# Kernel optimization log

Measured on AMD Instinct MI355X. Metric: run time of the kernel, lower is better.

Reference implementation:

```python
import jax, jax.numpy as jnp
import numpy as np

N = 100000
E = 1000000
F = 64
H = 64
G = 64  # number of graphs
EPS = 1e-5


def setup_inputs() -> dict:
    key = jax.random.key(0)
    ks = jax.random.split(key, 12)
    x = jax.random.normal(ks[0], (N, F), dtype=jnp.float32)
    edge_index = jax.random.randint(ks[1], (2, E), 0, N, dtype=jnp.int32)
    batch = jnp.sort(jax.random.randint(ks[2], (N,), 0, G, dtype=jnp.int32))
    s1 = 1.0 / np.sqrt(F)
    s2 = 1.0 / np.sqrt(H)
    inp = {
        "x": x,
        "edge_index": edge_index,
        "batch": batch,
        # GCNConv layers (weight [out,in] like torch Linear, bias [out])
        "W1": jax.random.uniform(ks[3], (H, F), jnp.float32, -s1, s1),
        "b1": jnp.zeros((H,), jnp.float32),
        "W2": jax.random.uniform(ks[4], (H, H), jnp.float32, -s2, s2),
        "b2": jnp.zeros((H,), jnp.float32),
        # BatchNorm (eval mode: running stats)
        "bn1_g": jnp.ones((H,), jnp.float32),
        "bn1_b": jnp.zeros((H,), jnp.float32),
        "bn1_m": jax.random.normal(ks[5], (H,), jnp.float32) * 0.1,
        "bn1_v": jax.random.uniform(ks[6], (H,), jnp.float32, 0.5, 1.5),
        "bn2_g": jnp.ones((H,), jnp.float32),
        "bn2_b": jnp.zeros((H,), jnp.float32),
        "bn2_m": jax.random.normal(ks[7], (H,), jnp.float32) * 0.1,
        "bn2_v": jax.random.uniform(ks[8], (H,), jnp.float32, 0.5, 1.5),
        # MLP head
        "lin1_W": jax.random.uniform(ks[9], (H // 2, H), jnp.float32, -s2, s2),
        "lin1_b": jnp.zeros((H // 2,), jnp.float32),
        "lin2_W": jax.random.uniform(ks[10], (1, H // 2), jnp.float32, -1.0 / np.sqrt(H // 2), 1.0 / np.sqrt(H // 2)),
        "lin2_b": jnp.zeros((1,), jnp.float32),
    }
    return inp


def _gcn_norm(edge_index):
    # PyG GCNConv default: add self-loops, symmetric normalization
    loop = jnp.arange(N, dtype=edge_index.dtype)
    row = jnp.concatenate([edge_index[0], loop])  # source
    col = jnp.concatenate([edge_index[1], loop])  # target
    deg = jax.ops.segment_sum(jnp.ones_like(col, jnp.float32), col, num_segments=N)
    dinv = jnp.where(deg > 0, jax.lax.rsqrt(deg), 0.0)
    norm = dinv[row] * dinv[col]  # [E+N]
    return row, col, norm


def _gcn_conv(x, W, b, row, col, norm):
    h = x @ W.T                       # [N, H] transform first (cheap)
    msg = h[row] * norm[:, None]      # [E+N, H] gather + scale
    out = jax.ops.segment_sum(msg, col, num_segments=N)  # scatter-add
    return out + b


def _bn_eval(x, g, b, m, v):
    return (x - m) * (g * jax.lax.rsqrt(v + EPS)) + b


def reference(x, edge_index, batch, W1, b1, W2, b2,
              bn1_g, bn1_b, bn1_m, bn1_v, bn2_g, bn2_b, bn2_m, bn2_v,
              lin1_W, lin1_b, lin2_W, lin2_b):
    row, col, norm = _gcn_norm(edge_index)
    # layer 1: conv -> BN -> relu (dropout inactive in eval)
    h = _gcn_conv(x, W1, b1, row, col, norm)
    h = jax.nn.relu(_bn_eval(h, bn1_g, bn1_b, bn1_m, bn1_v))
    # layer 2
    h = _gcn_conv(h, W2, b2, row, col, norm)
    h = jax.nn.relu(_bn_eval(h, bn2_g, bn2_b, bn2_m, bn2_v))
    # global mean pool over graphs
    sums = jax.ops.segment_sum(h, batch, num_segments=G)          # [G, H]
    cnt = jax.ops.segment_sum(jnp.ones((N,), h.dtype), batch, num_segments=G)
    pooled = sums / jnp.maximum(cnt, 1.0)[:, None]
    # MLP head
    z = jax.nn.relu(pooled @ lin1_W.T + lin1_b)
    return z @ lin2_W.T + lin2_b  # [G, 1]
```

## Files before the change

### kernel.cpp

```cpp
#include <hip/hip_runtime.h>
#include <math.h>

#define EPS_BN 1e-5f
#define CAP 48
#define BINSHIFT 9
#define EDGESHIFT 12
#define NBUCK_MAX 199

__device__ __forceinline__ float4 pull_fixed(const float4* __restrict__ h4, const int* __restrict__ icnt,
                                             const int* __restrict__ csr, int i, int q) {
    int deg = icnt[i];
    float di = rsqrtf((float)(deg + 1));
    float4 acc = h4[i * 16 + q];
    float dd = di * di;
    acc.x *= dd; acc.y *= dd; acc.z *= dd; acc.w *= dd;
    int degc = min(deg, CAP);
    int base = i * CAP;
    int kend = base + ((degc + 3) & ~3);
    for (int k = base; k < kend; k += 4) {
        int4 rr = *(const int4*)(csr + k);
        float w0 = rsqrtf((float)(icnt[rr.x] + 1)) * di;
        float w1 = rsqrtf((float)(icnt[rr.y] + 1)) * di;
        float w2 = rsqrtf((float)(icnt[rr.z] + 1)) * di;
        float w3 = rsqrtf((float)(icnt[rr.w] + 1)) * di;
        float4 v0 = h4[rr.x * 16 + q];
        float4 v1 = h4[rr.y * 16 + q];
        float4 v2 = h4[rr.z * 16 + q];
        float4 v3 = h4[rr.w * 16 + q];
        acc.x += v0.x * w0 + v1.x * w1 + v2.x * w2 + v3.x * w3;
        acc.y += v0.y * w0 + v1.y * w1 + v2.y * w2 + v3.y * w3;
        acc.z += v0.z * w0 + v1.z * w1 + v2.z * w2 + v3.z * w3;
        acc.w += v0.w * w0 + v1.w * w1 + v2.w * w2 + v3.w * w3;
    }
    return acc;
}

__device__ __forceinline__ float4 pull_plain(const float4* __restrict__ h4, const int* __restrict__ icnt,
                                             const int* __restrict__ csr, int i, int q) {
    int deg = icnt[i];
    float4 acc = h4[i * 16 + q];
    int degc = min(deg, CAP);
    int base = i * CAP;
    int kend = base + ((degc + 3) & ~3);
    for (int k = base; k < kend; k += 4) {
        int4 rr = *(const int4*)(csr + k);
        float4 v0 = h4[rr.x * 16 + q];
        float4 v1 = h4[rr.y * 16 + q];
        float4 v2 = h4[rr.z * 16 + q];
        float4 v3 = h4[rr.w * 16 + q];
        acc.x += v0.x + v1.x + v2.x + v3.x;
        acc.y += v0.y + v1.y + v2.y + v3.y;
        acc.z += v0.z + v1.z + v2.z + v3.z;
        acc.w += v0.w + v1.w + v2.w + v3.w;
    }
    float di = rsqrtf((float)(deg + 1));
    acc.x *= di; acc.y *= di; acc.z *= di; acc.w *= di;
    return acc;
}

template <bool ACT, bool SCALE>
__device__ __forceinline__ void gemm_tile128(const float4* __restrict__ in4, float4* sx, const float4* Wl,
                                             const float4* scl, const float4* shl,
                                             const int* __restrict__ icnt,
                                             float4* __restrict__ out4, int n, int tile, int tid) {
    int rbase = tile * 128;
#pragma unroll
    for (int k = 0; k < 8; ++k) {
        int idx = tid + k * 256;
        int r = idx >> 4, c = idx & 15;
        int gr = rbase + r;
        float4 v = (gr < n) ? in4[gr * 16 + c] : float4{0.f, 0.f, 0.f, 0.f};
        sx[(r << 4) | (c ^ ((r >> 1) & 15))] = v;
    }
    __syncthreads();

    int hg = tid >> 6;
    int h0 = hg * 16;
    int ng = tid & 63;
    int n0 = rbase + 2 * ng;
    int sw = ng & 15;
    float acc[2][16];
#pragma unroll
    for (int j = 0; j < 2; ++j)
#pragma unroll
        for (int k = 0; k < 16; ++k) acc[j][k] = 0.0f;

    for (int f4 = 0; f4 < 16; ++f4) {
        float4 sc, sh;
        if (ACT) { sc = scl[f4]; sh = shl[f4]; }
        float4 xv[2];
#pragma unroll
        for (int j = 0; j < 2; ++j) {
            float4 v = sx[((2 * ng + j) << 4) | (f4 ^ sw)];
            if (ACT) {
                v.x = fmaxf(v.x * sc.x + sh.x, 0.0f);
                v.y = fmaxf(v.y * sc.y + sh.y, 0.0f);
                v.z = fmaxf(v.z * sc.z + sh.z, 0.0f);
                v.w = fmaxf(v.w * sc.w + sh.w, 0.0f);
            }
            xv[j] = v;
        }
#pragma unroll
        for (int hh = 0; hh < 16; ++hh) {
            float4 w = Wl[(h0 + hh) * 16 + f4];
#pragma unroll
            for (int j = 0; j < 2; ++j) {
                acc[j][hh] += xv[j].x * w.x;
                acc[j][hh] += xv[j].y * w.y;
                acc[j][hh] += xv[j].z * w.z;
                acc[j][hh] += xv[j].w * w.w;
            }
        }
    }
#pragma unroll
    for (int j = 0; j < 2; ++j) {
        if (n0 + j >= n) continue;
        float di = 1.0f;
        if (SCALE) di = rsqrtf((float)(icnt[n0 + j] + 1));
#pragma unroll
        for (int q = 0; q < 4; ++q) {
            float4 o = {acc[j][4 * q] * di, acc[j][4 * q + 1] * di,
                        acc[j][4 * q + 2] * di, acc[j][4 * q + 3] * di};
            out4[(n0 + j) * 16 + (h0 >> 2) + q] = o;
        }
    }
}

__global__ __launch_bounds__(256) void k_init_f(int* icnt, float* gsum, float* gcnt,
    float* rowA, float* rowB, int n,
    const float* b1, const float* g1, const float* bb1, const float* m1, const float* v1,
    const float* b2, const float* g2, const float* bb2, const float* m2, const float* v2,
    float* sc1, float* sh1, float* sc2, float* sh2) {
    int gtid = blockIdx.x * 256 + threadIdx.x;
    if (gtid < 4096) gsum[gtid] = 0.0f;
    if (gtid < 64) { gcnt[gtid] = 0.0f; rowA[gtid] = 0.0f; rowB[gtid] = 0.0f; }
    if (gtid >= 64 && gtid < 68) icnt[n + gtid - 64] = 0;
    if (blockIdx.x == 0 && threadIdx.x < 64) {
        int t = threadIdx.x;
        float s1 = g1[t] / sqrtf(v1[t] + EPS_BN);
        sc1[t] = s1;
        sh1[t] = (b1[t] - m1[t]) * s1 + bb1[t];
        float s2 = g2[t] / sqrtf(v2[t] + EPS_BN);
        sc2[t] = s2;
        sh2[t] = (b2[t] - m2[t]) * s2 + bb2[t];
    }
}

__global__ __launch_bounds__(256) void k_gemm1bin(int nbg,
    const float* __restrict__ in, const float* __restrict__ W, float* __restrict__ out, int n,
    const int* __restrict__ row, const int* __restrict__ col, int e, int nbuck,
    int2* __restrict__ regions, int* __restrict__ offs) {
    __shared__ __align__(16) char smem[49152];
    int t = threadIdx.x;
    if ((int)blockIdx.x < nbg) {
        float4* sx = (float4*)smem;
        float4* Wl = (float4*)(smem + 32768);
        const float4* W4 = (const float4*)W;
        for (int i = t; i < 1024; i += 256) Wl[i] = W4[i];
        gemm_tile128<false, false>((const float4*)in, sx, Wl, nullptr, nullptr, nullptr,
                                   (float4*)out, n, blockIdx.x, t);
    } else {
        int2* so = (int2*)smem;
        int* soff = (int*)(smem + 32768);
        int* sfill = soff + 256;
        int blk = blockIdx.x - nbg;
        int base = blk << EDGESHIFT;
        int nE = min(1 << EDGESHIFT, e - base);

        int r4[16], c4[16];
        int j0 = t * 16;
        int m = nE - j0; m = m < 0 ? 0 : (m > 16 ? 16 : m);
        if (m == 16) {
#pragma unroll
            for (int cc = 0; cc < 4; ++cc) {
                int4 a = *(const int4*)(row + base + j0 + 4 * cc);
                int4 b = *(const int4*)(col + base + j0 + 4 * cc);
                r4[4 * cc] = a.x; r4[4 * cc + 1] = a.y; r4[4 * cc + 2] = a.z; r4[4 * cc + 3] = a.w;
                c4[4 * cc] = b.x; c4[4 * cc + 1] = b.y; c4[4 * cc + 2] = b.z; c4[4 * cc + 3] = b.w;
            }
        } else {
            for (int j = 0; j < m; ++j) { r4[j] = row[base + j0 + j]; c4[j] = col[base + j0 + j]; }
        }
        if (t < nbuck) { soff[t] = 0; sfill[t] = 0; }
        __syncthreads();
        for (int j = 0; j < m; ++j) atomicAdd(&soff[c4[j] >> BINSHIFT], 1);
        __syncthreads();
        for (int d = 1; d < nbuck; d <<= 1) {
            int add = 0;
            if (t < nbuck && t >= d) add = soff[t - d];
            __syncthreads();
            if (t < nbuck) soff[t] += add;
            __syncthreads();
        }
        for (int j = 0; j < m; ++j) {
            int bk = c4[j] >> BINSHIFT;
            int pos = (bk ? soff[bk - 1] : 0) + atomicAdd(&sfill[bk], 1);
            so[pos] = make_int2(r4[j], c4[j]);
        }
        __syncthreads();
        int4* gdst = (int4*)(regions + ((size_t)blk << EDGESHIFT));
        const int4* lsrc = (const int4*)so;
#pragma unroll
        for (int k = 0; k < 8; ++k) gdst[t + 256 * k] = lsrc[t + 256 * k];
        if (t <= nbuck) offs[blk * 200 + t] = (t == 0) ? 0 : soff[t - 1];
    }
}

__global__ __launch_bounds__(256) void k_build_f(
    const int2* __restrict__ regions, const int* __restrict__ offs, int nba, int n,
    int* __restrict__ icnt, int* __restrict__ csr) {
    __shared__ __align__(16) char smem[50176];
    int blk = blockIdx.x;
    int b = blk >> 1, s = blk & 1;
    int node0 = (b << BINSHIFT) + s * 256;
    if (node0 >= n) return;
    int* lcsr = (int*)smem;
    int* lcnt = (int*)(smem + 256 * CAP * 4);
    int t = threadIdx.x;
    for (int idx = t; idx < 256 * CAP; idx += 256) lcsr[idx] = n;
    lcnt[t] = 0;
    __syncthreads();
    for (int r = t; r < nba; r += 256) {
        int o0 = offs[r * 200 + b];
        int o1 = offs[r * 200 + b + 1];
        const int2* reg = regions + ((size_t)r << EDGESHIFT);
        for (int k = o0; k < o1; ++k) {
            int2 eg = reg[k];
            unsigned c = (unsigned)(eg.y - node0);
            if (c < 256u) {
                int u = atomicAdd(&lcnt[c], 1);
                if (u < CAP) lcsr[c * CAP + u] = eg.x;
            }
        }
    }
    __syncthreads();
    int nv = min(256, n - node0);
    for (int idx = t; idx < nv * CAP; idx += 256) csr[(size_t)node0 * CAP + idx] = lcsr[idx];
    if (t < nv) icnt[node0 + t] = lcnt[t];
}

__global__ __launch_bounds__(256) void k_apply_f(const float* __restrict__ h, const int* __restrict__ icnt,
                                                 const int* __restrict__ csr, float* __restrict__ out, int n) {
    int gid = blockIdx.x * 256 + threadIdx.x;
    int i = gid >> 4, q = gid & 15;
    if (i >= n) return;
    float4 acc = pull_fixed((const float4*)h, icnt, csr, i, q);
    ((float4*)out)[i * 16 + q] = acc;
}

__global__ __launch_bounds__(256) void k_gemm2s(const float* __restrict__ in, const float* __restrict__ W,
                                                const float* __restrict__ scale, const float* __restrict__ shift,
                                                const int* __restrict__ icnt,
                                                float* __restrict__ out, int n) {
    __shared__ __align__(16) char smem[49664];
    float4* sx = (float4*)smem;
    float4* Wl = (float4*)(smem + 32768);
    float4* scl = (float4*)(smem + 49152);
    float4* shl = scl + 16;
    const float4* W4 = (const float4*)W;
    for (int i = threadIdx.x; i < 1024; i += 256) Wl[i] = W4[i];
    if (threadIdx.x < 16) {
        scl[threadIdx.x] = ((const float4*)scale)[threadIdx.x];
        shl[threadIdx.x] = ((const float4*)shift)[threadIdx.x];
    }
    gemm_tile128<true, true>((const float4*)in, sx, Wl, scl, shl, icnt,
                             (float4*)out, n, blockIdx.x, threadIdx.x);
}

__global__ __launch_bounds__(256) void k_applypool_f(
    const float* __restrict__ h, const int* __restrict__ icnt, const int* __restrict__ csr,
    const int* __restrict__ batch,
    const float* __restrict__ sc, const float* __restrict__ sh,
    float* gsum, float* gcnt, int n) {
    __shared__ float spart[64 * 64];
    __shared__ float scnt[64];
    int node0 = blockIdx.x * 128;
    int last = min(node0 + 127, n - 1);
    int g0 = batch[node0];
    int rc = batch[last] - g0 + 1;
    for (int idx = threadIdx.x; idx < rc * 64; idx += 256) spart[idx] = 0.0f;
    if (threadIdx.x < rc) scnt[threadIdx.x] = 0.0f;
    __syncthreads();
    int q = threadIdx.x & 15;
    float4 s4 = ((const float4*)sc)[q];
    float4 b4 = ((const float4*)sh)[q];
    for (int it = 0; it < 8; ++it) {
        int i = node0 + it * 16 + (threadIdx.x >> 4);
        if (i < n) {
            float4 acc = pull_plain((const float4*)h, icnt, csr, i, q);
            acc.x = fmaxf(acc.x * s4.x + b4.x, 0.0f);
            acc.y = fmaxf(acc.y * s4.y + b4.y, 0.0f);
            acc.z = fmaxf(acc.z * s4.z + b4.z, 0.0f);
            acc.w = fmaxf(acc.w * s4.w + b4.w, 0.0f);
            int gl = batch[i] - g0;
            float* pp = &spart[gl * 64 + q * 4];
            atomicAdd(pp + 0, acc.x);
            atomicAdd(pp + 1, acc.y);
            atomicAdd(pp + 2, acc.z);
            atomicAdd(pp + 3, acc.w);
            if (q == 0) atomicAdd(&scnt[gl], 1.0f);
        }
    }
    __syncthreads();
    for (int idx = threadIdx.x; idx < rc * 64; idx += 256) {
        int gl = idx >> 6, f = idx & 63;
        atomicAdd(&gsum[(g0 + gl) * 64 + f], spart[idx]);
    }
    if (threadIdx.x < rc) atomicAdd(&gcnt[g0 + threadIdx.x], scnt[threadIdx.x]);
}

__global__ void k_mlp(const float* __restrict__ gsum, const float* __restrict__ gcnt,
                      const float* __restrict__ l1W, const float* __restrict__ l1b,
                      const float* __restrict__ l2W, const float* __restrict__ l2b,
                      float* __restrict__ outp) {
    int g = threadIdx.x;
    if (g >= 64) return;
    float inv = 1.0f / fmaxf(gcnt[g], 1.0f);
    float p[64];
#pragma unroll
    for (int hh = 0; hh < 64; ++hh) p[hh] = gsum[g * 64 + hh] * inv;
    float o = l2b[0];
    for (int j = 0; j < 32; ++j) {
        float a = l1b[j];
#pragma unroll
        for (int hh = 0; hh < 64; ++hh) a += p[hh] * l1W[j * 64 + hh];
        o += fmaxf(a, 0.0f) * l2W[j];
    }
    outp[g] = o;
}

extern "C" void kernel_launch(void* const* d_in, const int* in_sizes, int n_in,
                              void* d_out, int out_size, void* d_ws, size_t ws_size,
                              hipStream_t stream) {
    const int N = in_sizes[0] / 64;
    const int E = in_sizes[1] / 2;

    const float* x    = (const float*)d_in[0];
    const int*  row   = (const int*)d_in[1];
    const int*  colp  = ((const int*)d_in[1]) + E;
    const int*  batch = (const int*)d_in[2];
    const float* W1   = (const float*)d_in[3];
    const float* b1   = (const float*)d_in[4];
    const float* W2   = (const float*)d_in[5];
    const float* b2   = (const float*)d_in[6];
    const float* bn1g = (const float*)d_in[7];
    const float* bn1b = (const float*)d_in[8];
    const float* bn1m = (const float*)d_in[9];
    const float* bn1v = (const float*)d_in[10];
    const float* bn2g = (const float*)d_in[11];
    const float* bn2b = (const float*)d_in[12];
    const float* bn2m = (const float*)d_in[13];
    const float* bn2v = (const float*)d_in[14];
    const float* l1W  = (const float*)d_in[15];
    const float* l1b  = (const float*)d_in[16];
    const float* l2W  = (const float*)d_in[17];
    const float* l2b  = (const float*)d_in[18];
    float* out = (float*)d_out;

    int* icnt = (int*)d_ws;
    float* sc1 = (float*)(icnt + N + 4);
    float* sh1 = sc1 + 64;
    float* sc2 = sh1 + 64;
    float* sh2 = sc2 + 64;
    float* gsum = sh2 + 64;
    float* gcnt = gsum + 4096;
    int* csr = (int*)(gcnt + 64);
    float* bufA = (float*)(csr + (size_t)N * CAP);
    float* bufB = bufA + (size_t)(N + 1) * 64;

    const int NBLKA = (E + (1 << EDGESHIFT) - 1) >> EDGESHIFT;
    const int NBUCK = (N + 511) >> BINSHIFT;
    int2* regions = (int2*)bufB;
    int* offs = (int*)(regions + ((size_t)NBLKA << EDGESHIFT));

    int nbg     = (N + 127) / 128;
    int nb_n16  = (N * 16 + 255) / 256;
    int nb_apl  = (N + 127) / 128;
    int nbuild  = NBUCK * 2;

    k_init_f<<<16, 256, 0, stream>>>(icnt, gsum, gcnt,
                                     bufA + (size_t)N * 64, bufB + (size_t)N * 64, N,
                                     b1, bn1g, bn1b, bn1m, bn1v,
                                     b2, bn2g, bn2b, bn2m, bn2v,
                                     sc1, sh1, sc2, sh2);
    k_gemm1bin<<<nbg + NBLKA, 256, 0, stream>>>(nbg, x, W1, bufA, N,
                                                row, colp, E, NBUCK, regions, offs);
    k_build_f<<<nbuild, 256, 0, stream>>>(regions, offs, NBLKA, N, icnt, csr);
    k_apply_f<<<nb_n16, 256, 0, stream>>>(bufA, icnt, csr, bufB, N);
    k_gemm2s<<<nbg, 256, 0, stream>>>(bufB, W2, sc1, sh1, icnt, bufA, N);
    k_applypool_f<<<nb_apl, 256, 0, stream>>>(bufA, icnt, csr, batch, sc2, sh2, gsum, gcnt, N);
    k_mlp<<<1, 64, 0, stream>>>(gsum, gcnt, l1W, l1b, l2W, l2b, out);
}
```

Baseline: 320.9 us.

## Precompute dinv array, prefetch CSR indices, and split build/pool over more blocks

The build kernel now stores a per-node dinv (rsqrt of degree+1), so the pull kernels read one float instead of recomputing rsqrt from neighbor counts. The CSR index and region edge loops prefetch the next entry one step ahead. The build kernel splits each 512-node bucket into four 128-node blocks instead of two, and the pooling kernel uses 64 nodes per block, both to raise the block count and occupancy. The cost is more passes over region offsets in build (each block rescans every region for its bucket), an extra N-float array, and more global atomics in pooling.

```diff
diff --git a/kernel.cpp b/kernel.cpp
--- a/kernel.cpp
+++ b/kernel.cpp
@@ -7,53 +7,63 @@
 #define EDGESHIFT 12
 #define NBUCK_MAX 199
 
-__device__ __forceinline__ float4 pull_fixed(const float4* __restrict__ h4, const int* __restrict__ icnt,
-                                             const int* __restrict__ csr, int i, int q) {
+__device__ __forceinline__ float4 pull_fixed_d(const float4* __restrict__ h4, const float* __restrict__ dinv,
+                                               const int* __restrict__ icnt, const int* __restrict__ csr,
+                                               int i, int q) {
     int deg = icnt[i];
-    float di = rsqrtf((float)(deg + 1));
+    float di = dinv[i];
     float4 acc = h4[i * 16 + q];
     float dd = di * di;
     acc.x *= dd; acc.y *= dd; acc.z *= dd; acc.w *= dd;
     int degc = min(deg, CAP);
     int base = i * CAP;
     int kend = base + ((degc + 3) & ~3);
-    for (int k = base; k < kend; k += 4) {
-        int4 rr = *(const int4*)(csr + k);
-        float w0 = rsqrtf((float)(icnt[rr.x] + 1)) * di;
-        float w1 = rsqrtf((float)(icnt[rr.y] + 1)) * di;
-        float w2 = rsqrtf((float)(icnt[rr.z] + 1)) * di;
-        float w3 = rsqrtf((float)(icnt[rr.w] + 1)) * di;
-        float4 v0 = h4[rr.x * 16 + q];
-        float4 v1 = h4[rr.y * 16 + q];
-        float4 v2 = h4[rr.z * 16 + q];
-        float4 v3 = h4[rr.w * 16 + q];
-        acc.x += v0.x * w0 + v1.x * w1 + v2.x * w2 + v3.x * w3;
-        acc.y += v0.y * w0 + v1.y * w1 + v2.y * w2 + v3.y * w3;
-        acc.z += v0.z * w0 + v1.z * w1 + v2.z * w2 + v3.z * w3;
-        acc.w += v0.w * w0 + v1.w * w1 + v2.w * w2 + v3.w * w3;
+    if (base < kend) {
+        int4 rr = *(const int4*)(csr + base);
+        for (int k = base; k < kend; k += 4) {
+            int4 cur = rr;
+            if (k + 4 < kend) rr = *(const int4*)(csr + k + 4);
+            float w0 = dinv[cur.x] * di;
+            float w1 = dinv[cur.y] * di;
+            float w2 = dinv[cur.z] * di;
+            float w3 = dinv[cur.w] * di;
+            float4 v0 = h4[cur.x * 16 + q];
+            float4 v1 = h4[cur.y * 16 + q];
+            float4 v2 = h4[cur.z * 16 + q];
+            float4 v3 = h4[cur.w * 16 + q];
+            acc.x += v0.x * w0 + v1.x * w1 + v2.x * w2 + v3.x * w3;
+            acc.y += v0.y * w0 + v1.y * w1 + v2.y * w2 + v3.y * w3;
+            acc.z += v0.z * w0 + v1.z * w1 + v2.z * w2 + v3.z * w3;
+            acc.w += v0.w * w0 + v1.w * w1 + v2.w * w2 + v3.w * w3;
+        }
     }
     return acc;
 }
 
-__device__ __forceinline__ float4 pull_plain(const float4* __restrict__ h4, const int* __restrict__ icnt,
-                                             const int* __restrict__ csr, int i, int q) {
+__device__ __forceinline__ float4 pull_plain_d(const float4* __restrict__ h4, const int* __restrict__ icnt,
+                                               const float* __restrict__ dinv,
+                                               const int* __restrict__ csr, int i, int q) {
     int deg = icnt[i];
     float4 acc = h4[i * 16 + q];
     int degc = min(deg, CAP);
     int base = i * CAP;
     int kend = base + ((degc + 3) & ~3);
-    for (int k = base; k < kend; k += 4) {
-        int4 rr = *(const int4*)(csr + k);
-        float4 v0 = h4[rr.x * 16 + q];
-        float4 v1 = h4[rr.y * 16 + q];
-        float4 v2 = h4[rr.z * 16 + q];
-        float4 v3 = h4[rr.w * 16 + q];
-        acc.x += v0.x + v1.x + v2.x + v3.x;
-        acc.y += v0.y + v1.y + v2.y + v3.y;
-        acc.z += v0.z + v1.z + v2.z + v3.z;
-        acc.w += v0.w + v1.w + v2.w + v3.w;
-    }
-    float di = rsqrtf((float)(deg + 1));
+    if (base < kend) {
+        int4 rr = *(const int4*)(csr + base);
+        for (int k = base; k < kend; k += 4) {
+            int4 cur = rr;
+            if (k + 4 < kend) rr = *(const int4*)(csr + k + 4);
+            float4 v0 = h4[cur.x * 16 + q];
+            float4 v1 = h4[cur.y * 16 + q];
+            float4 v2 = h4[cur.z * 16 + q];
+            float4 v3 = h4[cur.w * 16 + q];
+            acc.x += v0.x + v1.x + v2.x + v3.x;
+            acc.y += v0.y + v1.y + v2.y + v3.y;
+            acc.z += v0.z + v1.z + v2.z + v3.z;
+            acc.w += v0.w + v1.w + v2.w + v3.w;
+        }
+    }
+    float di = dinv[i];
     acc.x *= di; acc.y *= di; acc.z *= di; acc.w *= di;
     return acc;
 }
@@ -126,7 +136,7 @@
     }
 }
 
-__global__ __launch_bounds__(256) void k_init_f(int* icnt, float* gsum, float* gcnt,
+__global__ __launch_bounds__(256) void k_init_f(int* icnt, float* dinv, float* gsum, float* gcnt,
     float* rowA, float* rowB, int n,
     const float* b1, const float* g1, const float* bb1, const float* m1, const float* v1,
     const float* b2, const float* g2, const float* bb2, const float* m2, const float* v2,
@@ -135,6 +145,7 @@
     if (gtid < 4096) gsum[gtid] = 0.0f;
     if (gtid < 64) { gcnt[gtid] = 0.0f; rowA[gtid] = 0.0f; rowB[gtid] = 0.0f; }
     if (gtid >= 64 && gtid < 68) icnt[n + gtid - 64] = 0;
+    if (gtid >= 68 && gtid < 72) dinv[n + gtid - 68] = 1.0f;
     if (blockIdx.x == 0 && threadIdx.x < 64) {
         int t = threadIdx.x;
         float s1 = g1[t] / sqrtf(v1[t] + EPS_BN);
@@ -208,43 +219,51 @@
 
 __global__ __launch_bounds__(256) void k_build_f(
     const int2* __restrict__ regions, const int* __restrict__ offs, int nba, int n,
-    int* __restrict__ icnt, int* __restrict__ csr) {
-    __shared__ __align__(16) char smem[50176];
+    int* __restrict__ icnt, float* __restrict__ dinv, int* __restrict__ csr) {
+    __shared__ int lcsr[128 * CAP];
+    __shared__ int lcnt[128];
     int blk = blockIdx.x;
-    int b = blk >> 1, s = blk & 1;
-    int node0 = (b << BINSHIFT) + s * 256;
+    int b = blk >> 2, s = blk & 3;
+    int node0 = (b << BINSHIFT) + s * 128;
     if (node0 >= n) return;
-    int* lcsr = (int*)smem;
-    int* lcnt = (int*)(smem + 256 * CAP * 4);
     int t = threadIdx.x;
-    for (int idx = t; idx < 256 * CAP; idx += 256) lcsr[idx] = n;
-    lcnt[t] = 0;
+    for (int idx = t; idx < 128 * CAP; idx += 256) lcsr[idx] = n;
+    if (t < 128) lcnt[t] = 0;
     __syncthreads();
     for (int r = t; r < nba; r += 256) {
         int o0 = offs[r * 200 + b];
         int o1 = offs[r * 200 + b + 1];
         const int2* reg = regions + ((size_t)r << EDGESHIFT);
-        for (int k = o0; k < o1; ++k) {
-            int2 eg = reg[k];
-            unsigned c = (unsigned)(eg.y - node0);
-            if (c < 256u) {
-                int u = atomicAdd(&lcnt[c], 1);
-                if (u < CAP) lcsr[c * CAP + u] = eg.x;
+        if (o0 < o1) {
+            int2 eg = reg[o0];
+            for (int k = o0; k < o1; ++k) {
+                int2 cur = eg;
+                if (k + 1 < o1) eg = reg[k + 1];
+                unsigned c = (unsigned)(cur.y - node0);
+                if (c < 128u) {
+                    int u = atomicAdd(&lcnt[c], 1);
+                    if (u < CAP) lcsr[c * CAP + u] = cur.x;
+                }
             }
         }
     }
     __syncthreads();
-    int nv = min(256, n - node0);
+    int nv = min(128, n - node0);
     for (int idx = t; idx < nv * CAP; idx += 256) csr[(size_t)node0 * CAP + idx] = lcsr[idx];
-    if (t < nv) icnt[node0 + t] = lcnt[t];
+    if (t < nv) {
+        int d = lcnt[t];
+        icnt[node0 + t] = d;
+        dinv[node0 + t] = rsqrtf((float)(d + 1));
+    }
 }
 
 __global__ __launch_bounds__(256) void k_apply_f(const float* __restrict__ h, const int* __restrict__ icnt,
+                                                 const float* __restrict__ dinv,
                                                  const int* __restrict__ csr, float* __restrict__ out, int n) {
     int gid = blockIdx.x * 256 + threadIdx.x;
     int i = gid >> 4, q = gid & 15;
     if (i >= n) return;
-    float4 acc = pull_fixed((const float4*)h, icnt, csr, i, q);
+    float4 acc = pull_fixed_d((const float4*)h, dinv, icnt, csr, i, q);
     ((float4*)out)[i * 16 + q] = acc;
 }
 
@@ -268,14 +287,14 @@
 }
 
 __global__ __launch_bounds__(256) void k_applypool_f(
-    const float* __restrict__ h, const int* __restrict__ icnt, const int* __restrict__ csr,
-    const int* __restrict__ batch,
+    const float* __restrict__ h, const int* __restrict__ icnt, const float* __restrict__ dinv,
+    const int* __restrict__ csr, const int* __restrict__ batch,
     const float* __restrict__ sc, const float* __restrict__ sh,
     float* gsum, float* gcnt, int n) {
     __shared__ float spart[64 * 64];
     __shared__ float scnt[64];
-    int node0 = blockIdx.x * 128;
-    int last = min(node0 + 127, n - 1);
+    int node0 = blockIdx.x * 64;
+    int last = min(node0 + 63, n - 1);
     int g0 = batch[node0];
     int rc = batch[last] - g0 + 1;
     for (int idx = threadIdx.x; idx < rc * 64; idx += 256) spart[idx] = 0.0f;
@@ -284,10 +303,10 @@
     int q = threadIdx.x & 15;
     float4 s4 = ((const float4*)sc)[q];
     float4 b4 = ((const float4*)sh)[q];
-    for (int it = 0; it < 8; ++it) {
+    for (int it = 0; it < 4; ++it) {
         int i = node0 + it * 16 + (threadIdx.x >> 4);
         if (i < n) {
-            float4 acc = pull_plain((const float4*)h, icnt, csr, i, q);
+            float4 acc = pull_plain_d((const float4*)h, icnt, dinv, csr, i, q);
             acc.x = fmaxf(acc.x * s4.x + b4.x, 0.0f);
             acc.y = fmaxf(acc.y * s4.y + b4.y, 0.0f);
             acc.z = fmaxf(acc.z * s4.z + b4.z, 0.0f);
@@ -358,7 +377,8 @@
     float* out = (float*)d_out;
 
     int* icnt = (int*)d_ws;
-    float* sc1 = (float*)(icnt + N + 4);
+    float* dinv = (float*)(icnt + N + 4);
+    float* sc1 = dinv + N + 4;
     float* sh1 = sc1 + 64;
     float* sc2 = sh1 + 64;
     float* sh2 = sc2 + 64;
@@ -375,19 +395,19 @@
 
     int nbg     = (N + 127) / 128;
     int nb_n16  = (N * 16 + 255) / 256;
-    int nb_apl  = (N + 127) / 128;
-    int nbuild  = NBUCK * 2;
-
-    k_init_f<<<16, 256, 0, stream>>>(icnt, gsum, gcnt,
+    int nb_apl  = (N + 63) / 64;
+    int nbuild  = NBUCK * 4;
+
+    k_init_f<<<16, 256, 0, stream>>>(icnt, dinv, gsum, gcnt,
                                      bufA + (size_t)N * 64, bufB + (size_t)N * 64, N,
                                      b1, bn1g, bn1b, bn1m, bn1v,
                                      b2, bn2g, bn2b, bn2m, bn2v,
                                      sc1, sh1, sc2, sh2);
     k_gemm1bin<<<nbg + NBLKA, 256, 0, stream>>>(nbg, x, W1, bufA, N,
                                                 row, colp, E, NBUCK, regions, offs);
-    k_build_f<<<nbuild, 256, 0, stream>>>(regions, offs, NBLKA, N, icnt, csr);
-    k_apply_f<<<nb_n16, 256, 0, stream>>>(bufA, icnt, csr, bufB, N);
+    k_build_f<<<nbuild, 256, 0, stream>>>(regions, offs, NBLKA, N, icnt, dinv, csr);
+    k_apply_f<<<nb_n16, 256, 0, stream>>>(bufA, icnt, dinv, csr, bufB, N);
     k_gemm2s<<<nbg, 256, 0, stream>>>(bufB, W2, sc1, sh1, icnt, bufA, N);
-    k_applypool_f<<<nb_apl, 256, 0, stream>>>(bufA, icnt, csr, batch, sc2, sh2, gsum, gcnt, N);
+    k_applypool_f<<<nb_apl, 256, 0, stream>>>(bufA, icnt, dinv, csr, batch, sc2, sh2, gsum, gcnt, N);
     k_mlp<<<1, 64, 0, stream>>>(gsum, gcnt, l1W, l1b, l2W, l2b, out);
 }
```

After: 328.7 us. +2.4%, slower.
